# Kernel optimization log

Measured on AMD Instinct MI355X. Metric: run time of the kernel, lower is better.

## Reference

```python
import jax, jax.numpy as jnp
import numpy as np

N = 10000       # nodes (cells)
NFEAT = 2000    # gene-expression features
NFE = 256       # embed features
NH = 128        # nhid
NHE = 64        # nhid_embed
L = 2           # gcn_hid_layers_num
NOUT = 20       # output classes
BN_EPS = 1e-5


def bn_eval(x, g, b, rm, rv):
    # BatchNorm1d in eval mode: affine with running stats
    return g * (x - rm) / jnp.sqrt(rv + BN_EPS) + b


def lstm_layer(seq, Wih, Whh, bih, bhh):
    # seq: [T, N, H_in]; PyTorch gate order i, f, g, o
    Hd = Whh.shape[1]
    def step(carry, xt):
        h, c = carry
        z = xt @ Wih.T + h @ Whh.T + bih + bhh  # [N, 4H]
        i, f, g, o = jnp.split(z, 4, axis=1)
        c = jax.nn.sigmoid(f) * c + jax.nn.sigmoid(i) * jnp.tanh(g)
        h = jax.nn.sigmoid(o) * jnp.tanh(c)
        return (h, c), h
    h0 = jnp.zeros((seq.shape[1], Hd), seq.dtype)
    _, hs = jax.lax.scan(step, (h0, h0), seq)
    return hs  # [T, N, H]


def setup_inputs() -> dict:
    key = jax.random.key(0)
    ks = iter(jax.random.split(key, 48))
    def rn(shape, scale=1.0):
        return jax.random.normal(next(ks), shape, dtype=jnp.float32) * scale
    inp = {}
    inp["x"] = rn((N, NFEAT))
    inp["embed"] = rn((N, NFE))
    inp["adj"] = jax.random.uniform(next(ks), (N, N), dtype=jnp.float32)
    inp["W_in"] = rn((NH, NFEAT), NFEAT ** -0.5); inp["b_in"] = jnp.zeros((NH,), jnp.float32)
    inp["bn_in_g"] = jnp.ones((NH,), jnp.float32); inp["bn_in_b"] = jnp.zeros((NH,), jnp.float32)
    inp["bn_in_rm"] = rn((NH,), 0.1); inp["bn_in_rv"] = jnp.ones((NH,), jnp.float32)
    # gs_block: Linear(2*nhid -> nhid) per layer (concat self + mean-aggregated neighbors)
    inp["W_gs"] = rn((L, NH, 2 * NH), (2 * NH) ** -0.5); inp["b_gs"] = jnp.zeros((L, NH), jnp.float32)
    for l in range(2):  # 2-layer LSTM jumping-knowledge
        inp[f"Wih{l}"] = rn((4 * NH, NH), NH ** -0.5)
        inp[f"Whh{l}"] = rn((4 * NH, NH), NH ** -0.5)
        inp[f"bih{l}"] = jnp.zeros((4 * NH,), jnp.float32)
        inp[f"bhh{l}"] = jnp.zeros((4 * NH,), jnp.float32)
    inp["W_emb"] = rn((NHE, NFE), NFE ** -0.5); inp["b_emb"] = jnp.zeros((NHE,), jnp.float32)
    inp["bn_emb_g"] = jnp.ones((NHE,), jnp.float32); inp["bn_emb_b"] = jnp.zeros((NHE,), jnp.float32)
    inp["bn_emb_rm"] = rn((NHE,), 0.1); inp["bn_emb_rv"] = jnp.ones((NHE,), jnp.float32)
    D = NH + NHE
    inp["W_fc"] = rn((D, D), D ** -0.5); inp["b_fc"] = jnp.zeros((D,), jnp.float32)
    inp["bn_fc_g"] = jnp.ones((D,), jnp.float32); inp["bn_fc_b"] = jnp.zeros((D,), jnp.float32)
    inp["bn_fc_rm"] = rn((D,), 0.1); inp["bn_fc_rv"] = jnp.ones((D,), jnp.float32)
    inp["W_out"] = rn((NOUT, D), D ** -0.5); inp["b_out"] = jnp.zeros((NOUT,), jnp.float32)
    return inp


def _forward(x, embed, adj, W_in, b_in, bn_in_g, bn_in_b, bn_in_rm, bn_in_rv,
             W_gs, b_gs, Wih0, Whh0, bih0, bhh0, Wih1, Whh1, bih1, bhh1,
             W_emb, b_emb, bn_emb_g, bn_emb_b, bn_emb_rm, bn_emb_rv,
             W_fc, b_fc, bn_fc_g, bn_fc_b, bn_fc_rm, bn_fc_rv, W_out, b_out):
    # input projection + BN + ELU (dropout: eval mode -> no-op)
    h = jax.nn.elu(bn_eval(x @ W_in.T + b_in, bn_in_g, bn_in_b, bn_in_rm, bn_in_rv))
    # GraphSAGE mean aggregator: row-normalized dense adjacency
    adj_norm = adj / adj.sum(1, keepdims=True)
    jk = []
    for l in range(L):
        neigh = adj_norm @ h                              # [N, NH] neighbor mean
        comb = jnp.concatenate([h, neigh], axis=1)        # [N, 2NH] (gcn=False)
        h = jax.nn.relu(comb @ W_gs[l].T + b_gs[l])
        h = h / jnp.maximum(jnp.linalg.norm(h, axis=1, keepdims=True), 1e-12)  # F.normalize
        jk.append(h)
    seq = jnp.stack(jk, 0)                                # [L, N, NH]
    hs = lstm_layer(seq, Wih0, Whh0, bih0, bhh0)
    hs = lstm_layer(hs, Wih1, Whh1, bih1, bhh1)
    h = hs.mean(0)                                        # JK: mean of LSTM outputs
    h = jax.nn.elu(bn_eval(h, bn_in_g, bn_in_b, bn_in_rm, bn_in_rv))  # bn_node_in_exp reused
    e = jax.nn.elu(bn_eval(embed @ W_emb.T + b_emb, bn_emb_g, bn_emb_b, bn_emb_rm, bn_emb_rv))
    h = jnp.concatenate([h, e], axis=1)                   # [N, NH+NHE]
    h = jax.nn.elu(bn_eval(h @ W_fc.T + b_fc, bn_fc_g, bn_fc_b, bn_fc_rm, bn_fc_rv))
    logits = h @ W_out.T + b_out
    return jax.nn.log_softmax(logits, axis=1)


def reference(x, embed, adj, W_in, b_in, bn_in_g, bn_in_b, bn_in_rm, bn_in_rv,
              W_gs, b_gs, Wih0, Whh0, bih0, bhh0, Wih1, Whh1, bih1, bhh1,
              W_emb, b_emb, bn_emb_g, bn_emb_b, bn_emb_rm, bn_emb_rv,
              W_fc, b_fc, bn_fc_g, bn_fc_b, bn_fc_rm, bn_fc_rv, W_out, b_out):
    return _forward(x, embed, adj, W_in, b_in, bn_in_g, bn_in_b, bn_in_rm, bn_in_rv,
                    W_gs, b_gs, Wih0, Whh0, bih0, bhh0, Wih1, Whh1, bih1, bhh1,
                    W_emb, b_emb, bn_emb_g, bn_emb_b, bn_emb_rm, bn_emb_rv,
                    W_fc, b_fc, bn_fc_g, bn_fc_b, bn_fc_rm, bn_fc_rv, W_out, b_out)
```

## Files before the change

kernel.cpp:

```cpp
#include <hip/hip_runtime.h>
#include <hip/hip_bf16.h>
#include <math.h>

#define N_NODES 10000
#define NFEAT   2000
#define NFE     256
#define NH      128
#define NHE     64
#define NOUT    20
#define DCAT    192
#define BN_EPS  1e-5f

#define KP      10016
#define KSTEPS  313
#define MT      157
#define NSPLIT  8
#define KC      40
#define NSPLX   4
#define MPAD    10048

typedef __attribute__((ext_vector_type(8))) short  bf16x8;
typedef __attribute__((ext_vector_type(4))) float  f32x4;

__device__ __forceinline__ float sigm(float x) { return 1.0f / (1.0f + expf(-x)); }

__device__ __forceinline__ unsigned short f2bf(float x) {
    union { __hip_bfloat16 h; unsigned short u; } c;
    c.h = __float2bfloat16(x);
    return c.u;
}

__device__ __forceinline__ bf16x8 cvt8(const float* v) {
    bf16x8 r;
    #pragma unroll
    for (int i = 0; i < 8; ++i) r[i] = (short)f2bf(v[i]);
    return r;
}

__global__ __launch_bounds__(256) void wconv_kernel(const float* __restrict__ Wih0,
                                                    const float* __restrict__ Whh0,
                                                    const float* __restrict__ Wih1,
                                                    const float* __restrict__ Whh1,
                                                    const float* __restrict__ Wgs,
                                                    unsigned short* __restrict__ wl,
                                                    unsigned short* __restrict__ wgb)
{
    const int total = 262144 + 65536;
    for (int i = blockIdx.x * 256 + threadIdx.x; i < total; i += gridDim.x * 256) {
        if (i < 262144) {
            int l = i >> 17, rem = i & 131071;
            int n = rem >> 8, k = rem & 255;
            const float* src;
            if (l == 0) src = (k < 128) ? (Wih0 + n * 128 + k) : (Whh0 + n * 128 + (k - 128));
            else        src = (k < 128) ? (Wih1 + n * 128 + k) : (Whh1 + n * 128 + (k - 128));
            wl[i] = f2bf(*src);
        } else {
            int j = i - 262144;
            wgb[j] = f2bf(Wgs[j]);
        }
    }
}

__global__ __launch_bounds__(256) void adjmm_kernel(const float* __restrict__ adj,
                                                    const unsigned short* __restrict__ hT,
                                                    float* __restrict__ part,
                                                    float* __restrict__ part_s)
{
    __shared__ unsigned short sa[2][64 * 32];
    __shared__ unsigned short sb[2][128 * 32];
    const int tid  = threadIdx.x;
    const int lane = tid & 63, w = tid >> 6;
    const int m0   = blockIdx.x * 64;
    const int ks0  = blockIdx.y * KC;
    const int ks1  = min(ks0 + KC, KSTEPS);
    const int r0   = (w & 1) * 32;
    const int c0   = (w >> 1) * 64;

    const int arow = tid >> 2, agrp = tid & 3;
    const size_t abase = (size_t)min(m0 + arow, N_NODES - 1) * N_NODES;
    const int bcol = tid >> 1, bg0 = (tid & 1) * 2;

    const int asoff  = arow * 32 + ((agrp ^ (arow & 3)) << 3);
    const int bsoff0 = bcol * 32 + (((bg0 + 0) ^ (bcol & 3)) << 3);
    const int bsoff1 = bcol * 32 + (((bg0 + 1) ^ (bcol & 3)) << 3);

    float rs = 0.f;
    f32x4 acc[2][4];
    #pragma unroll
    for (int i = 0; i < 2; ++i)
        #pragma unroll
        for (int j = 0; j < 4; ++j) acc[i][j] = (f32x4){0.f, 0.f, 0.f, 0.f};

    float av8[8];
    bf16x8 vb0, vb1;
    auto load_step = [&](int ks) {
        const int k0 = ks * 32;
        const int kg = k0 + agrp * 8;
        if (kg + 8 <= N_NODES) {
            float4 u0 = *(const float4*)(adj + abase + kg);
            float4 u1 = *(const float4*)(adj + abase + kg + 4);
            av8[0] = u0.x; av8[1] = u0.y; av8[2] = u0.z; av8[3] = u0.w;
            av8[4] = u1.x; av8[5] = u1.y; av8[6] = u1.z; av8[7] = u1.w;
        } else {
            #pragma unroll
            for (int i = 0; i < 8; ++i) av8[i] = 0.f;
        }
        #pragma unroll
        for (int i = 0; i < 8; ++i) rs += av8[i];
        vb0 = *(const bf16x8*)(hT + (size_t)bcol * KP + k0 + bg0 * 8);
        vb1 = *(const bf16x8*)(hT + (size_t)bcol * KP + k0 + (bg0 + 1) * 8);
    };
    auto write_step = [&](int p) {
        *(bf16x8*)(sa[p] + asoff)  = cvt8(av8);
        *(bf16x8*)(sb[p] + bsoff0) = vb0;
        *(bf16x8*)(sb[p] + bsoff1) = vb1;
    };

    load_step(ks0);
    write_step(0);

    for (int ks = ks0; ks < ks1; ++ks) {
        const int p = (ks - ks0) & 1;
        const bool more = (ks + 1 < ks1);
        if (more) load_step(ks + 1);
        __syncthreads();
        bf16x8 av[2], bv[4];
        #pragma unroll
        for (int rb = 0; rb < 2; ++rb) {
            int row = r0 + rb * 16 + (lane & 15);
            int g   = lane >> 4;
            av[rb] = *(const bf16x8*)(sa[p] + row * 32 + ((g ^ (row & 3)) << 3));
        }
        #pragma unroll
        for (int cb = 0; cb < 4; ++cb) {
            int col = c0 + cb * 16 + (lane & 15);
            int g   = lane >> 4;
            bv[cb] = *(const bf16x8*)(sb[p] + col * 32 + ((g ^ (col & 3)) << 3));
        }
        #pragma unroll
        for (int rb = 0; rb < 2; ++rb)
            #pragma unroll
            for (int cb = 0; cb < 4; ++cb)
                acc[rb][cb] = __builtin_amdgcn_mfma_f32_16x16x32_bf16(av[rb], bv[cb],
                                                                      acc[rb][cb], 0, 0, 0);
        if (more) write_step(p ^ 1);
    }

    rs += __shfl_xor(rs, 1);
    rs += __shfl_xor(rs, 2);
    if ((tid & 3) == 0) part_s[(size_t)blockIdx.y * MPAD + m0 + arow] = rs;

    float* pout = part + (size_t)blockIdx.y * MPAD * NH;
    #pragma unroll
    for (int rb = 0; rb < 2; ++rb)
        #pragma unroll
        for (int cb = 0; cb < 4; ++cb) {
            int rowb = m0 + r0 + rb * 16 + (lane >> 4) * 4;
            int col  = c0 + cb * 16 + (lane & 15);
            #pragma unroll
            for (int reg = 0; reg < 4; ++reg)
                pout[(size_t)(rowb + reg) * NH + col] = acc[rb][cb][reg];
        }
}

__global__ __launch_bounds__(256) void xw_mfma_kernel(const float* __restrict__ x,
                                                      const float* __restrict__ Wn,
                                                      float* __restrict__ part)
{
    __shared__ unsigned short sa[2][64 * 32];
    __shared__ unsigned short sb[2][128 * 32];
    const int tid  = threadIdx.x;
    const int lane = tid & 63, w = tid >> 6;
    const int m0   = blockIdx.x * 64;
    const int TOT  = (NFEAT + 31) / 32;
    const int s0   = blockIdx.y * 16;
    const int s1   = min(s0 + 16, TOT);
    const int r0   = (w & 1) * 32;
    const int c0   = (w >> 1) * 64;

    const int arow = tid >> 2, agrp = tid & 3;
    const size_t abase = (size_t)min(m0 + arow, N_NODES - 1) * NFEAT;
    const int asoff = arow * 32 + ((agrp ^ (arow & 3)) << 3);
    const int bn0 = tid >> 2;
    int bn_[2], bgrp_[2], bsoff_[2];
    #pragma unroll
    for (int t = 0; t < 2; ++t) {
        int gi = tid + t * 256;
        bn_[t] = gi >> 2; bgrp_[t] = gi & 3;
        bsoff_[t] = bn_[t] * 32 + ((bgrp_[t] ^ (bn_[t] & 3)) << 3);
    }

    f32x4 acc[2][4];
    #pragma unroll
    for (int i = 0; i < 2; ++i)
        #pragma unroll
        for (int j = 0; j < 4; ++j) acc[i][j] = (f32x4){0.f, 0.f, 0.f, 0.f};

    float av8[8], bv8[2][8];
    auto load_step = [&](int ks) {
        const int k0 = ks * 32;
        {
            const int kg = k0 + agrp * 8;
            if (kg + 8 <= NFEAT) {
                float4 u0 = *(const float4*)(x + abase + kg);
                float4 u1 = *(const float4*)(x + abase + kg + 4);
                av8[0]=u0.x; av8[1]=u0.y; av8[2]=u0.z; av8[3]=u0.w;
                av8[4]=u1.x; av8[5]=u1.y; av8[6]=u1.z; av8[7]=u1.w;
            } else {
                #pragma unroll
                for (int i = 0; i < 8; ++i) av8[i] = 0.f;
            }
        }
        #pragma unroll
        for (int t = 0; t < 2; ++t) {
            int kg = k0 + bgrp_[t] * 8;
            if (kg + 8 <= NFEAT) {
                float4 u0 = *(const float4*)(Wn + (size_t)bn_[t] * NFEAT + kg);
                float4 u1 = *(const float4*)(Wn + (size_t)bn_[t] * NFEAT + kg + 4);
                bv8[t][0]=u0.x; bv8[t][1]=u0.y; bv8[t][2]=u0.z; bv8[t][3]=u0.w;
                bv8[t][4]=u1.x; bv8[t][5]=u1.y; bv8[t][6]=u1.z; bv8[t][7]=u1.w;
            } else {
                #pragma unroll
                for (int i = 0; i < 8; ++i) bv8[t][i] = 0.f;
            }
        }
    };
    auto write_step = [&](int p) {
        *(bf16x8*)(sa[p] + asoff) = cvt8(av8);
        #pragma unroll
        for (int t = 0; t < 2; ++t)
            *(bf16x8*)(sb[p] + bsoff_[t]) = cvt8(bv8[t]);
    };

    load_step(s0);
    write_step(0);

    for (int ks = s0; ks < s1; ++ks) {
        const int p = (ks - s0) & 1;
        const bool more = (ks + 1 < s1);
        if (more) load_step(ks + 1);
        __syncthreads();
        bf16x8 av[2], bv[4];
        #pragma unroll
        for (int rb = 0; rb < 2; ++rb) {
            int row = r0 + rb * 16 + (lane & 15);
            int g   = lane >> 4;
            av[rb] = *(const bf16x8*)(sa[p] + row * 32 + ((g ^ (row & 3)) << 3));
        }
        #pragma unroll
        for (int cb = 0; cb < 4; ++cb) {
            int col = c0 + cb * 16 + (lane & 15);
            int g   = lane >> 4;
            bv[cb] = *(const bf16x8*)(sb[p] + col * 32 + ((g ^ (col & 3)) << 3));
        }
        #pragma unroll
        for (int rb = 0; rb < 2; ++rb)
            #pragma unroll
            for (int cb = 0; cb < 4; ++cb)
                acc[rb][cb] = __builtin_amdgcn_mfma_f32_16x16x32_bf16(av[rb], bv[cb],
                                                                      acc[rb][cb], 0, 0, 0);
        if (more) write_step(p ^ 1);
    }
    float* pout = part + (size_t)blockIdx.y * MPAD * NH;
    #pragma unroll
    for (int rb = 0; rb < 2; ++rb)
        #pragma unroll
        for (int cb = 0; cb < 4; ++cb) {
            int rowb = m0 + r0 + rb * 16 + (lane >> 4) * 4;
            int col  = c0 + cb * 16 + (lane & 15);
            #pragma unroll
            for (int reg = 0; reg < 4; ++reg)
                pout[(size_t)(rowb + reg) * NH + col] = acc[rb][cb][reg];
        }
}

__global__ __launch_bounds__(256) void xw_reduce_kernel(const float* __restrict__ part,
                                                        const float* __restrict__ bias,
                                                        const float* __restrict__ g,
                                                        const float* __restrict__ bb,
                                                        const float* __restrict__ rm,
                                                        const float* __restrict__ rv,
                                                        float* __restrict__ h,
                                                        unsigned short* __restrict__ hT)
{
    __shared__ unsigned short tb[128][8];
    const int tid = threadIdx.x;
    int idx = blockIdx.x * 256 + tid;
    const int c4 = (tid & 31) * 4;
    const int lr = tid >> 5;
    const int m0g = blockIdx.x * 8;
    const size_t ch = (size_t)MPAD * NH / 4;
    const float4* p = (const float4*)part;
    float a[4] = {0.f, 0.f, 0.f, 0.f};
    #pragma unroll
    for (int c = 0; c < NSPLX; ++c) {
        float4 v = p[c * ch + idx];
        a[0] += v.x; a[1] += v.y; a[2] += v.z; a[3] += v.w;
    }
    float o[4];
    #pragma unroll
    for (int j = 0; j < 4; ++j) {
        int c = c4 + j;
        float sc = g[c] / sqrtf(rv[c] + BN_EPS);
        float t = (a[j] + bias[c] - rm[c]) * sc + bb[c];
        o[j] = t > 0.f ? t : expm1f(t);
        tb[c][lr] = f2bf(o[j]);
    }
    float4 ov; ov.x = o[0]; ov.y = o[1]; ov.z = o[2]; ov.w = o[3];
    *(float4*)(h + (size_t)idx * 4) = ov;
    __syncthreads();
    if (tid < 128) {
        ushort4 v0, v1;
        v0.x = tb[tid][0]; v0.y = tb[tid][1]; v0.z = tb[tid][2]; v0.w = tb[tid][3];
        v1.x = tb[tid][4]; v1.y = tb[tid][5]; v1.z = tb[tid][6]; v1.w = tb[tid][7];
        *(ushort4*)(hT + (size_t)tid * KP + m0g)     = v0;
        *(ushort4*)(hT + (size_t)tid * KP + m0g + 4) = v1;
        if (blockIdx.x == 0) {
            ushort4 zz; zz.x = zz.y = zz.z = zz.w = 0;
            #pragma unroll
            for (int q = 0; q < 4; ++q)
                *(ushort4*)(hT + (size_t)tid * KP + 10000 + q * 4) = zz;
        }
    }
}

template<bool WRITE_T>
__global__ __launch_bounds__(256) void gs_fused_kernel(const float* __restrict__ h,
                                                       const float* __restrict__ part,
                                                       const float* __restrict__ part_s,
                                                       const unsigned short* __restrict__ Wg,
                                                       const float* __restrict__ bg,
                                                       float* __restrict__ jk,
                                                       unsigned short* __restrict__ jkT)
{
    __shared__ unsigned short sa[64 * 32];
    __shared__ unsigned short sb[128 * 32];
    __shared__ float ssq_l[64][2];
    __shared__ unsigned short tb[WRITE_T ? 128 * 64 : 1];
    const int tid  = threadIdx.x;
    const int lane = tid & 63, w = tid >> 6;
    const int m0   = blockIdx.x * 64;
    const int r0   = (w & 1) * 32;
    const int c0   = (w >> 1) * 64;
    const int arow = tid >> 2, agrp = tid & 3;
    const int mg   = min(m0 + arow, N_NODES - 1);

    float inv;
    {
        float s = 0.f;
        #pragma unroll
        for (int c = 0; c < NSPLIT; ++c) s += part_s[(size_t)c * MPAD + mg];
        inv = 1.0f / s;
    }

    f32x4 acc[2][4];
    #pragma unroll
    for (int i = 0; i < 2; ++i)
        #pragma unroll
        for (int j = 0; j < 4; ++j) acc[i][j] = (f32x4){0.f, 0.f, 0.f, 0.f};

    for (int k0 = 0; k0 < 256; k0 += 32) {
        const int kg = k0 + agrp * 8;
        float a8[8];
        if (kg < 128) {
            const float* asrc = h + (size_t)mg * NH + kg;
            float4 u0 = *(const float4*)asrc;
            float4 u1 = *(const float4*)(asrc + 4);
            a8[0]=u0.x; a8[1]=u0.y; a8[2]=u0.z; a8[3]=u0.w;
            a8[4]=u1.x; a8[5]=u1.y; a8[6]=u1.z; a8[7]=u1.w;
        } else {
            const int cc = kg - 128;
            float s0x=0,s0y=0,s0z=0,s0w=0,s1x=0,s1y=0,s1z=0,s1w=0;
            #pragma unroll
            for (int c = 0; c < NSPLIT; ++c) {
                const float* pp = part + (size_t)c * MPAD * NH + (size_t)mg * NH + cc;
                float4 v0 = *(const float4*)pp;
                float4 v1 = *(const float4*)(pp + 4);
                s0x+=v0.x; s0y+=v0.y; s0z+=v0.z; s0w+=v0.w;
                s1x+=v1.x; s1y+=v1.y; s1z+=v1.z; s1w+=v1.w;
            }
            a8[0]=s0x*inv; a8[1]=s0y*inv; a8[2]=s0z*inv; a8[3]=s0w*inv;
            a8[4]=s1x*inv; a8[5]=s1y*inv; a8[6]=s1z*inv; a8[7]=s1w*inv;
        }
        bf16x8 b8[2];
        #pragma unroll
        for (int t = 0; t < 2; ++t) {
            int gi = tid + t * 256;
            int n = gi >> 2, grp = gi & 3;
            b8[t] = *(const bf16x8*)(Wg + (size_t)n * 256 + k0 + grp * 8);
        }
        __syncthreads();
        *(bf16x8*)(sa + arow * 32 + ((agrp ^ (arow & 3)) << 3)) = cvt8(a8);
        #pragma unroll
        for (int t = 0; t < 2; ++t) {
            int gi = tid + t * 256;
            int n = gi >> 2, grp = gi & 3;
            *(bf16x8*)(sb + n * 32 + ((grp ^ (n & 3)) << 3)) = b8[t];
        }
        __syncthreads();
        bf16x8 av[2], bv[4];
        #pragma unroll
        for (int rb = 0; rb < 2; ++rb) {
            int row = r0 + rb * 16 + (lane & 15);
            int g   = lane >> 4;
            av[rb] = *(const bf16x8*)(sa + row * 32 + ((g ^ (row & 3)) << 3));
        }
        #pragma unroll
        for (int cb = 0; cb < 4; ++cb) {
            int col = c0 + cb * 16 + (lane & 15);
            int g   = lane >> 4;
            bv[cb] = *(const bf16x8*)(sb + col * 32 + ((g ^ (col & 3)) << 3));
        }
        #pragma unroll
        for (int rb = 0; rb < 2; ++rb)
            #pragma unroll
            for (int cb = 0; cb < 4; ++cb)
                acc[rb][cb] = __builtin_amdgcn_mfma_f32_16x16x32_bf16(av[rb], bv[cb],
                                                                      acc[rb][cb], 0, 0, 0);
    }

    float vv[2][4][4];
    float ps[2][4] = {};
    #pragma unroll
    for (int rb = 0; rb < 2; ++rb)
        #pragma unroll
        for (int cb = 0; cb < 4; ++cb) {
            int colg = c0 + cb * 16 + (lane & 15);
            float b = bg[colg];
            #pragma unroll
            for (int reg = 0; reg < 4; ++reg) {
                float t = fmaxf(acc[rb][cb][reg] + b, 0.f);
                vv[rb][cb][reg] = t;
                ps[rb][reg] += t * t;
            }
        }
    #pragma unroll
    for (int msk = 1; msk < 16; msk <<= 1)
        #pragma unroll
        for (int rb = 0; rb < 2; ++rb)
            #pragma unroll
            for (int reg = 0; reg < 4; ++reg)
                ps[rb][reg] += __shfl_xor(ps[rb][reg], msk);
    if ((lane & 15) == 0) {
        #pragma unroll
        for (int rb = 0; rb < 2; ++rb)
            #pragma unroll
            for (int reg = 0; reg < 4; ++reg)
                ssq_l[r0 + rb * 16 + (lane >> 4) * 4 + reg][w >> 1] = ps[rb][reg];
    }
    __syncthreads();
    #pragma unroll
    for (int rb = 0; rb < 2; ++rb)
        #pragma unroll
        for (int reg = 0; reg < 4; ++reg) {
            int lr = r0 + rb * 16 + (lane >> 4) * 4 + reg;
            float s = ssq_l[lr][0] + ssq_l[lr][1];
            float sc = 1.0f / fmaxf(sqrtf(s), 1e-12f);
            int m = m0 + lr;
            #pragma unroll
            for (int cb = 0; cb < 4; ++cb) {
                int colg = c0 + cb * 16 + (lane & 15);
                float o = vv[rb][cb][reg] * sc;
                if (m < N_NODES) jk[(size_t)m * NH + colg] = o;
                if constexpr (WRITE_T) tb[colg * 64 + lr] = f2bf(o);
            }
        }
    if constexpr (WRITE_T) {
        __syncthreads();
        #pragma unroll
        for (int p = 0; p < 4; ++p) {
            int flat = (tid + p * 256) * 8;
            int c = flat >> 6, mo = flat & 63;
            int kglob = m0 + mo;
            if (kglob < KP) {
                unsigned short tmp[8];
                #pragma unroll
                for (int i = 0; i < 8; ++i)
                    tmp[i] = (kglob + i < N_NODES) ? tb[c * 64 + mo + i] : (unsigned short)0;
                ushort4 v0, v1;
                v0.x = tmp[0]; v0.y = tmp[1]; v0.z = tmp[2]; v0.w = tmp[3];
                v1.x = tmp[4]; v1.y = tmp[5]; v1.z = tmp[6]; v1.w = tmp[7];
                *(ushort4*)(jkT + (size_t)c * KP + kglob)     = v0;
                *(ushort4*)(jkT + (size_t)c * KP + kglob + 4) = v1;
            }
        }
    }
}

template<bool HASC, bool FINAL>
__global__ __launch_bounds__(256) void lstm_fused_kernel(
    int K, const float* __restrict__ a1, const float* __restrict__ a2,
    const unsigned short* __restrict__ wl,
    const float* __restrict__ bih, const float* __restrict__ bhh,
    const float* __restrict__ cprev,
    float* __restrict__ hout, float* __restrict__ cout,
    const float* __restrict__ hmean, const float* __restrict__ bng,
    const float* __restrict__ bnb, const float* __restrict__ bnrm,
    const float* __restrict__ bnrv, float* __restrict__ hpost)
{
    __shared__ unsigned short sa[32 * 32];
    __shared__ unsigned short sb[512 * 32];
    const int tid  = threadIdx.x;
    const int lane = tid & 63, w = tid >> 6;
    const int m0   = blockIdx.x * 32;
    const int arow = tid >> 2, agrp = tid & 3;
    const int mg   = min(m0 + arow, N_NODES - 1);

    f32x4 acc[2][8];
    #pragma unroll
    for (int i = 0; i < 2; ++i)
        #pragma unroll
        for (int j = 0; j < 8; ++j) acc[i][j] = (f32x4){0.f, 0.f, 0.f, 0.f};

    for (int k0 = 0; k0 < K; k0 += 32) {
        float a8[8];
        if (tid < 128) {
            int kg = k0 + agrp * 8;
            const float* asrc = (kg < 128) ? (a1 + (size_t)mg * NH + kg)
                                           : (a2 + (size_t)mg * NH + (kg - 128));
            float4 u0 = *(const float4*)asrc;
            float4 u1 = *(const float4*)(asrc + 4);
            a8[0]=u0.x; a8[1]=u0.y; a8[2]=u0.z; a8[3]=u0.w;
            a8[4]=u1.x; a8[5]=u1.y; a8[6]=u1.z; a8[7]=u1.w;
        }
        bf16x8 b8[8];
        #pragma unroll
        for (int t = 0; t < 8; ++t) {
            int gi = tid + t * 256;
            int n = gi >> 2, grp = gi & 3;
            b8[t] = *(const bf16x8*)(wl + (size_t)n * 256 + k0 + grp * 8);
        }
        __syncthreads();
        if (tid < 128)
            *(bf16x8*)(sa + arow * 32 + ((agrp ^ (arow & 3)) << 3)) = cvt8(a8);
        #pragma unroll
        for (int t = 0; t < 8; ++t) {
            int gi = tid + t * 256;
            int n = gi >> 2, grp = gi & 3;
            *(bf16x8*)(sb + n * 32 + ((grp ^ (n & 3)) << 3)) = b8[t];
        }
        __syncthreads();
        bf16x8 av[2];
        #pragma unroll
        for (int rb = 0; rb < 2; ++rb) {
            int row = rb * 16 + (lane & 15);
            int g   = lane >> 4;
            av[rb] = *(const bf16x8*)(sa + row * 32 + ((g ^ (row & 3)) << 3));
        }
        #pragma unroll
        for (int gate = 0; gate < 4; ++gate)
            #pragma unroll
            for (int cb = 0; cb < 2; ++cb) {
                int col = gate * 128 + w * 32 + cb * 16 + (lane & 15);
                int g   = lane >> 4;
                bf16x8 bv = *(const bf16x8*)(sb + col * 32 + ((g ^ (col & 3)) << 3));
                #pragma unroll
                for (int rb = 0; rb < 2; ++rb)
                    acc[rb][gate * 2 + cb] =
                        __builtin_amdgcn_mfma_f32_16x16x32_bf16(av[rb], bv,
                                                                acc[rb][gate * 2 + cb], 0, 0, 0);
            }
    }

    #pragma unroll
    for (int cb = 0; cb < 2; ++cb) {
        const int cg = w * 32 + cb * 16 + (lane & 15);
        const float bi = bih[0 * 128 + cg] + bhh[0 * 128 + cg];
        const float bf = bih[1 * 128 + cg] + bhh[1 * 128 + cg];
        const float bgg= bih[2 * 128 + cg] + bhh[2 * 128 + cg];
        const float bo = bih[3 * 128 + cg] + bhh[3 * 128 + cg];
        float sc = 0.f, sh = 0.f;
        if constexpr (FINAL) {
            sc = bng[cg] / sqrtf(bnrv[cg] + BN_EPS);
            sh = bnb[cg] - bnrm[cg] * sc;
        }
        #pragma unroll
        for (int rb = 0; rb < 2; ++rb) {
            #pragma unroll
            for (int reg = 0; reg < 4; ++reg) {
                int m = m0 + rb * 16 + (lane >> 4) * 4 + reg;
                if (m < N_NODES) {
                    float zi = acc[rb][0 + cb][reg] + bi;
                    float zf = acc[rb][2 + cb][reg] + bf;
                    float zg = acc[rb][4 + cb][reg] + bgg;
                    float zo = acc[rb][6 + cb][reg] + bo;
                    float cn = sigm(zi) * tanhf(zg);
                    if constexpr (HASC) cn += sigm(zf) * cprev[(size_t)m * NH + cg];
                    float hv = sigm(zo) * tanhf(cn);
                    if constexpr (FINAL) {
                        float t = 0.5f * (hmean[(size_t)m * NH + cg] + hv);
                        t = t * sc + sh;
                        hpost[(size_t)m * NH + cg] = t > 0.f ? t : expm1f(t);
                    } else {
                        hout[(size_t)m * NH + cg] = hv;
                        cout[(size_t)m * NH + cg] = cn;
                    }
                }
            }
        }
    }
}

template<int BM, int BN>
__global__ __launch_bounds__(256) void wgemm_bnelu_kernel(
    int M, int K, int kSplitA,
    const float* __restrict__ a1, int lda1,
    const float* __restrict__ a2, int lda2,
    const float* __restrict__ B, int ldb, int ncol,
    float* __restrict__ out, int ldo,
    const float* __restrict__ bias,
    const float* __restrict__ bng, const float* __restrict__ bnb,
    const float* __restrict__ bnrm, const float* __restrict__ bnrv)
{
    constexpr int WC = BN / 64;
    constexpr int WR = 4 / WC;
    static_assert(WR * WC == 4 && BM == WR * 32, "geometry");
    constexpr int NGA = BM * 4 / 256;
    constexpr int NGB = BN * 4 / 256;
    __shared__ unsigned short sa[BM * 32];
    __shared__ unsigned short sb[BN * 32];
    const int tid  = threadIdx.x;
    const int lane = tid & 63, w = tid >> 6;
    const int m0   = blockIdx.x * BM, n0 = blockIdx.y * BN;
    const int r0   = (w % WR) * 32, c0 = (w / WR) * 64;

    f32x4 acc[2][4];
    #pragma unroll
    for (int i = 0; i < 2; ++i)
        #pragma unroll
        for (int j = 0; j < 4; ++j) acc[i][j] = (f32x4){0.f, 0.f, 0.f, 0.f};

    for (int k0 = 0; k0 < K; k0 += 32) {
        float ar[NGA][8], br[NGB][8];
        #pragma unroll
        for (int t = 0; t < NGA; ++t) {
            int gi = tid + t * 256;
            int row = gi >> 2, grp = gi & 3;
            int mg = min(m0 + row, M - 1);
            int kg = k0 + grp * 8;
            const float* src = (kg < kSplitA) ? (a1 + (size_t)mg * lda1 + kg)
                                              : (a2 + (size_t)mg * lda2 + (kg - kSplitA));
            float4 u0 = *(const float4*)src;
            float4 u1 = *(const float4*)(src + 4);
            ar[t][0]=u0.x; ar[t][1]=u0.y; ar[t][2]=u0.z; ar[t][3]=u0.w;
            ar[t][4]=u1.x; ar[t][5]=u1.y; ar[t][6]=u1.z; ar[t][7]=u1.w;
        }
        #pragma unroll
        for (int t = 0; t < NGB; ++t) {
            int gi = tid + t * 256;
            int n = gi >> 2, grp = gi & 3;
            int ng = min(n0 + n, ncol - 1);
            int kg = k0 + grp * 8;
            const float* src = B + (size_t)ng * ldb + kg;
            float4 u0 = *(const float4*)src;
            float4 u1 = *(const float4*)(src + 4);
            br[t][0]=u0.x; br[t][1]=u0.y; br[t][2]=u0.z; br[t][3]=u0.w;
            br[t][4]=u1.x; br[t][5]=u1.y; br[t][6]=u1.z; br[t][7]=u1.w;
        }
        __syncthreads();
        #pragma unroll
        for (int t = 0; t < NGA; ++t) {
            int gi = tid + t * 256;
            int row = gi >> 2, grp = gi & 3;
            *(bf16x8*)(sa + row * 32 + ((grp ^ (row & 3)) << 3)) = cvt8(ar[t]);
        }
        #pragma unroll
        for (int t = 0; t < NGB; ++t) {
            int gi = tid + t * 256;
            int n = gi >> 2, grp = gi & 3;
            *(bf16x8*)(sb + n * 32 + ((grp ^ (n & 3)) << 3)) = cvt8(br[t]);
        }
        __syncthreads();
        bf16x8 av[2], bv[4];
        #pragma unroll
        for (int rb = 0; rb < 2; ++rb) {
            int row = r0 + rb * 16 + (lane & 15);
            int g   = lane >> 4;
            av[rb] = *(const bf16x8*)(sa + row * 32 + ((g ^ (row & 3)) << 3));
        }
        #pragma unroll
        for (int cb = 0; cb < 4; ++cb) {
            int col = c0 + cb * 16 + (lane & 15);
            int g   = lane >> 4;
            bv[cb] = *(const bf16x8*)(sb + col * 32 + ((g ^ (col & 3)) << 3));
        }
        #pragma unroll
        for (int rb = 0; rb < 2; ++rb)
            #pragma unroll
            for (int cb = 0; cb < 4; ++cb)
                acc[rb][cb] = __builtin_amdgcn_mfma_f32_16x16x32_bf16(av[rb], bv[cb],
                                                                      acc[rb][cb], 0, 0, 0);
    }

    #pragma unroll
    for (int cb = 0; cb < 4; ++cb) {
        const int colg = n0 + c0 + cb * 16 + (lane & 15);
        const int cc = min(colg, ncol - 1);
        float badd = bias[cc];
        float sc = bng[cc] / sqrtf(bnrv[cc] + BN_EPS);
        float sh = bnb[cc] - bnrm[cc] * sc;
        #pragma unroll
        for (int rb = 0; rb < 2; ++rb) {
            int rowb = m0 + r0 + rb * 16 + (lane >> 4) * 4;
            #pragma unroll
            for (int reg = 0; reg < 4; ++reg) {
                int m = rowb + reg;
                if (m < M && colg < ncol) {
                    float t = (acc[rb][cb][reg] + badd) * sc + sh;
                    out[(size_t)m * ldo + colg] = t > 0.f ? t : expm1f(t);
                }
            }
        }
    }
}

__global__ __launch_bounds__(256) void out_kernel(const float* __restrict__ hfc,
                                                  const float* __restrict__ W_out,
                                                  const float* __restrict__ b_out,
                                                  float* __restrict__ out)
{
    __shared__ float wl[NOUT * 193];
    __shared__ float rl[4][DCAT];
    const int tid = threadIdx.x;
    for (int i = tid; i < NOUT * DCAT; i += 256)
        wl[(i / DCAT) * 193 + (i % DCAT)] = W_out[i];
    const int w = tid >> 6, lane = tid & 63;
    const int r = blockIdx.x * 4 + w;
    for (int k = lane; k < DCAT; k += 64) rl[w][k] = hfc[(size_t)r * DCAT + k];
    __syncthreads();
    const int c = lane;
    float acc = -INFINITY;
    if (c < NOUT) {
        acc = b_out[c];
        #pragma unroll 4
        for (int k = 0; k < DCAT; ++k) acc += rl[w][k] * wl[c * 193 + k];
    }
    float mx = acc;
    #pragma unroll
    for (int msk = 16; msk >= 1; msk >>= 1) mx = fmaxf(mx, __shfl_xor(mx, msk));
    float ex = (c < NOUT) ? expf(acc - mx) : 0.f;
    float sm = ex;
    #pragma unroll
    for (int msk = 16; msk >= 1; msk >>= 1) sm += __shfl_xor(sm, msk);
    if (c < NOUT) out[(size_t)r * NOUT + c] = acc - mx - logf(sm);
}

extern "C" void kernel_launch(void* const* d_in, const int* in_sizes, int n_in,
                              void* d_out, int out_size, void* d_ws, size_t ws_size,
                              hipStream_t stream)
{
    const float* x       = (const float*)d_in[0];
    const float* embed   = (const float*)d_in[1];
    const float* adj     = (const float*)d_in[2];
    const float* W_in    = (const float*)d_in[3];
    const float* b_in    = (const float*)d_in[4];
    const float* bn_in_g = (const float*)d_in[5];
    const float* bn_in_b = (const float*)d_in[6];
    const float* bn_in_rm= (const float*)d_in[7];
    const float* bn_in_rv= (const float*)d_in[8];
    const float* W_gs    = (const float*)d_in[9];
    const float* b_gs    = (const float*)d_in[10];
    const float* Wih0    = (const float*)d_in[11];
    const float* Whh0    = (const float*)d_in[12];
    const float* bih0    = (const float*)d_in[13];
    const float* bhh0    = (const float*)d_in[14];
    const float* Wih1    = (const float*)d_in[15];
    const float* Whh1    = (const float*)d_in[16];
    const float* bih1    = (const float*)d_in[17];
    const float* bhh1    = (const float*)d_in[18];
    const float* W_emb   = (const float*)d_in[19];
    const float* b_emb   = (const float*)d_in[20];
    const float* bn_e_g  = (const float*)d_in[21];
    const float* bn_e_b  = (const float*)d_in[22];
    const float* bn_e_rm = (const float*)d_in[23];
    const float* bn_e_rv = (const float*)d_in[24];
    const float* W_fc    = (const float*)d_in[25];
    const float* b_fc    = (const float*)d_in[26];
    const float* bn_f_g  = (const float*)d_in[27];
    const float* bn_f_b  = (const float*)d_in[28];
    const float* bn_f_rm = (const float*)d_in[29];
    const float* bn_f_rv = (const float*)d_in[30];
    const float* W_out   = (const float*)d_in[31];
    const float* b_out   = (const float*)d_in[32];
    float* outp = (float*)d_out;

    const size_t HB = (size_t)N_NODES * NH * sizeof(float);
    char* wp = (char*)d_ws;
    auto carve = [&](size_t bytes) {
        void* p = (void*)wp;
        wp += (bytes + 1023) & ~(size_t)1023;
        return p;
    };
    float* part  = (float*)carve((size_t)NSPLIT * MPAD * NH * sizeof(float));
    float* part_s= (float*)carve((size_t)NSPLIT * MPAD * sizeof(float));
    float* h_in  = (float*)carve(HB);
    float* jk0   = (float*)carve(HB);
    float* jk1   = (float*)carve(HB);
    float* h1_0  = (float*)carve(HB);
    float* h1_1  = (float*)carve(HB);
    float* c1    = (float*)carve(HB);
    float* h2_0  = (float*)carve(HB);
    float* c2    = (float*)carve(HB);
    float* hpost = (float*)carve(HB);
    float* e     = (float*)carve((size_t)N_NODES * NHE * sizeof(float));
    float* hfc   = (float*)carve((size_t)N_NODES * DCAT * sizeof(float));
    unsigned short* hT  = (unsigned short*)carve((size_t)NH * KP * 2);
    unsigned short* wl  = (unsigned short*)carve((size_t)2 * 512 * 256 * 2);
    unsigned short* wgb = (unsigned short*)carve((size_t)2 * 128 * 256 * 2);
    if ((size_t)(wp - (char*)d_ws) > ws_size) return;

    const dim3 blk(256);

    wconv_kernel<<<320, blk, 0, stream>>>(Wih0, Whh0, Wih1, Whh1, W_gs, wl, wgb);

    xw_mfma_kernel<<<dim3(MT, NSPLX), blk, 0, stream>>>(x, W_in, part);
    xw_reduce_kernel<<<1250, blk, 0, stream>>>(part, b_in, bn_in_g, bn_in_b,
                                               bn_in_rm, bn_in_rv, h_in, hT);

    adjmm_kernel<<<dim3(MT, NSPLIT), blk, 0, stream>>>(adj, hT, part, part_s);
    gs_fused_kernel<true><<<MT, blk, 0, stream>>>(h_in, part, part_s, wgb, b_gs, jk0, hT);

    adjmm_kernel<<<dim3(MT, NSPLIT), blk, 0, stream>>>(adj, hT, part, part_s);
    gs_fused_kernel<false><<<MT, blk, 0, stream>>>(jk0, part, part_s, wgb + 128 * 256,
                                                   b_gs + 128, jk1, nullptr);

    lstm_fused_kernel<false, false><<<313, blk, 0, stream>>>(
        128, jk0, jk0, wl, bih0, bhh0, nullptr, h1_0, c1,
        nullptr, nullptr, nullptr, nullptr, nullptr, nullptr);
    lstm_fused_kernel<true, false><<<313, blk, 0, stream>>>(
        256, jk1, h1_0, wl, bih0, bhh0, c1, h1_1, c1,
        nullptr, nullptr, nullptr, nullptr, nullptr, nullptr);
    lstm_fused_kernel<false, false><<<313, blk, 0, stream>>>(
        128, h1_0, h1_0, wl + 512 * 256, bih1, bhh1, nullptr, h2_0, c2,
        nullptr, nullptr, nullptr, nullptr, nullptr, nullptr);
    lstm_fused_kernel<true, true><<<313, blk, 0, stream>>>(
        256, h1_1, h2_0, wl + 512 * 256, bih1, bhh1, c2, nullptr, nullptr,
        h2_0, bn_in_g, bn_in_b, bn_in_rm, bn_in_rv, hpost);

    wgemm_bnelu_kernel<64, 128><<<dim3(MT, 1), blk, 0, stream>>>(
        N_NODES, NFE, NFE, embed, NFE, nullptr, 0,
        W_emb, NFE, NHE, e, NHE,
        b_emb, bn_e_g, bn_e_b, bn_e_rm, bn_e_rv);

    wgemm_bnelu_kernel<64, 128><<<dim3(MT, 2), blk, 0, stream>>>(
        N_NODES, DCAT, NH, hpost, NH, e, NHE,
        W_fc, DCAT, DCAT, hfc, DCAT,
        b_fc, bn_f_g, bn_f_b, bn_f_rm, bn_f_rv);

    out_kernel<<<2500, blk, 0, stream>>>(hfc, W_out, b_out, outp);
}
```

Before: 476.9 us.

## Fuse LSTM chain and epilogue GEMMs, store adj partials in bf16, double K-splits

The four LSTM step launches become one kernel that keeps hidden states in LDS as bf16 and cell states in registers, so the h/c intermediates no longer round-trip through global memory. The embed GEMM, FC GEMM and output log-softmax are merged into a single epilogue kernel. The adj-matmul split-K partials are now written in bf16 with twice as many K-splits, which halves the bytes per partial and raises parallelism. In exchange, partial sums are rounded to bf16 before reduction, which costs some precision, and the fused kernels use more shared memory, which may lower occupancy.

Measured after the change: 475.4 us. About the same (-0.3%).

```diff
diff --git a/kernel.cpp b/kernel.cpp
--- a/kernel.cpp
+++ b/kernel.cpp
@@ -14,8 +14,8 @@
 #define KP      10016
 #define KSTEPS  313
 #define MT      157
-#define NSPLIT  8
-#define KC      40
+#define NSPLIT  16
+#define KC      20
 #define NSPLX   4
 #define MPAD    10048
 
@@ -28,6 +28,12 @@
     union { __hip_bfloat16 h; unsigned short u; } c;
     c.h = __float2bfloat16(x);
     return c.u;
+}
+
+__device__ __forceinline__ float bf2f(unsigned short u) {
+    union { float f; unsigned int i; } c;
+    c.i = ((unsigned int)u) << 16;
+    return c.f;
 }
 
 __device__ __forceinline__ bf16x8 cvt8(const float* v) {
@@ -63,7 +69,7 @@
 
 __global__ __launch_bounds__(256) void adjmm_kernel(const float* __restrict__ adj,
                                                     const unsigned short* __restrict__ hT,
-                                                    float* __restrict__ part,
+                                                    unsigned short* __restrict__ part,
                                                     float* __restrict__ part_s)
 {
     __shared__ unsigned short sa[2][64 * 32];
@@ -105,12 +111,12 @@
             #pragma unroll
             for (int i = 0; i < 8; ++i) av8[i] = 0.f;
         }
-        #pragma unroll
-        for (int i = 0; i < 8; ++i) rs += av8[i];
         vb0 = *(const bf16x8*)(hT + (size_t)bcol * KP + k0 + bg0 * 8);
         vb1 = *(const bf16x8*)(hT + (size_t)bcol * KP + k0 + (bg0 + 1) * 8);
     };
     auto write_step = [&](int p) {
+        #pragma unroll
+        for (int i = 0; i < 8; ++i) rs += av8[i];
         *(bf16x8*)(sa[p] + asoff)  = cvt8(av8);
         *(bf16x8*)(sb[p] + bsoff0) = vb0;
         *(bf16x8*)(sb[p] + bsoff1) = vb1;
@@ -150,7 +156,7 @@
     rs += __shfl_xor(rs, 2);
     if ((tid & 3) == 0) part_s[(size_t)blockIdx.y * MPAD + m0 + arow] = rs;
 
-    float* pout = part + (size_t)blockIdx.y * MPAD * NH;
+    unsigned short* pout = part + (size_t)blockIdx.y * MPAD * NH;
     #pragma unroll
     for (int rb = 0; rb < 2; ++rb)
         #pragma unroll
@@ -159,7 +165,7 @@
             int col  = c0 + cb * 16 + (lane & 15);
             #pragma unroll
             for (int reg = 0; reg < 4; ++reg)
-                pout[(size_t)(rowb + reg) * NH + col] = acc[rb][cb][reg];
+                pout[(size_t)(rowb + reg) * NH + col] = f2bf(acc[rb][cb][reg]);
         }
 }
 
@@ -181,7 +187,6 @@
     const int arow = tid >> 2, agrp = tid & 3;
     const size_t abase = (size_t)min(m0 + arow, N_NODES - 1) * NFEAT;
     const int asoff = arow * 32 + ((agrp ^ (arow & 3)) << 3);
-    const int bn0 = tid >> 2;
     int bn_[2], bgrp_[2], bsoff_[2];
     #pragma unroll
     for (int t = 0; t < 2; ++t) {
@@ -326,7 +331,7 @@
 
 template<bool WRITE_T>
 __global__ __launch_bounds__(256) void gs_fused_kernel(const float* __restrict__ h,
-                                                       const float* __restrict__ part,
+                                                       const unsigned short* __restrict__ part,
                                                        const float* __restrict__ part_s,
                                                        const unsigned short* __restrict__ Wg,
                                                        const float* __restrict__ bg,
@@ -370,17 +375,15 @@
             a8[4]=u1.x; a8[5]=u1.y; a8[6]=u1.z; a8[7]=u1.w;
         } else {
             const int cc = kg - 128;
-            float s0x=0,s0y=0,s0z=0,s0w=0,s1x=0,s1y=0,s1z=0,s1w=0;
+            float s[8] = {0.f,0.f,0.f,0.f,0.f,0.f,0.f,0.f};
             #pragma unroll
             for (int c = 0; c < NSPLIT; ++c) {
-                const float* pp = part + (size_t)c * MPAD * NH + (size_t)mg * NH + cc;
-                float4 v0 = *(const float4*)pp;
-                float4 v1 = *(const float4*)(pp + 4);
-                s0x+=v0.x; s0y+=v0.y; s0z+=v0.z; s0w+=v0.w;
-                s1x+=v1.x; s1y+=v1.y; s1z+=v1.z; s1w+=v1.w;
-            }
-            a8[0]=s0x*inv; a8[1]=s0y*inv; a8[2]=s0z*inv; a8[3]=s0w*inv;
-            a8[4]=s1x*inv; a8[5]=s1y*inv; a8[6]=s1z*inv; a8[7]=s1w*inv;
+                bf16x8 v = *(const bf16x8*)(part + (size_t)c * MPAD * NH + (size_t)mg * NH + cc);
+                #pragma unroll
+                for (int i = 0; i < 8; ++i) s[i] += bf2f((unsigned short)v[i]);
+            }
+            #pragma unroll
+            for (int i = 0; i < 8; ++i) a8[i] = s[i] * inv;
         }
         bf16x8 b8[2];
         #pragma unroll
@@ -487,262 +490,335 @@
     }
 }
 
-template<bool HASC, bool FINAL>
-__global__ __launch_bounds__(256) void lstm_fused_kernel(
-    int K, const float* __restrict__ a1, const float* __restrict__ a2,
+__global__ __launch_bounds__(256) void lstm4_kernel(
+    const float* __restrict__ jk0, const float* __restrict__ jk1,
     const unsigned short* __restrict__ wl,
-    const float* __restrict__ bih, const float* __restrict__ bhh,
-    const float* __restrict__ cprev,
-    float* __restrict__ hout, float* __restrict__ cout,
-    const float* __restrict__ hmean, const float* __restrict__ bng,
-    const float* __restrict__ bnb, const float* __restrict__ bnrm,
-    const float* __restrict__ bnrv, float* __restrict__ hpost)
+    const float* __restrict__ bih0, const float* __restrict__ bhh0,
+    const float* __restrict__ bih1, const float* __restrict__ bhh1,
+    const float* __restrict__ bng, const float* __restrict__ bnb,
+    const float* __restrict__ bnrm, const float* __restrict__ bnrv,
+    float* __restrict__ hpost)
 {
     __shared__ unsigned short sa[32 * 32];
     __shared__ unsigned short sb[512 * 32];
-    const int tid  = threadIdx.x;
-    const int lane = tid & 63, w = tid >> 6;
-    const int m0   = blockIdx.x * 32;
+    __shared__ unsigned short hb[2][32][136];
+    const int tid = threadIdx.x, lane = tid & 63, w = tid >> 6;
+    const int m0 = blockIdx.x * 32;
     const int arow = tid >> 2, agrp = tid & 3;
-    const int mg   = min(m0 + arow, N_NODES - 1);
+    const int mg = min(m0 + arow, N_NODES - 1);
 
     f32x4 acc[2][8];
-    #pragma unroll
-    for (int i = 0; i < 2; ++i)
-        #pragma unroll
-        for (int j = 0; j < 8; ++j) acc[i][j] = (f32x4){0.f, 0.f, 0.f, 0.f};
-
-    for (int k0 = 0; k0 < K; k0 += 32) {
-        float a8[8];
+    float cst[2][2][4];
+
+    auto zacc = [&] {
+        #pragma unroll
+        for (int i = 0; i < 2; ++i)
+            #pragma unroll
+            for (int j = 0; j < 8; ++j) acc[i][j] = (f32x4){0.f, 0.f, 0.f, 0.f};
+    };
+    auto stage_sb = [&](const unsigned short* wlayer, int k0) {
+        #pragma unroll
+        for (int t = 0; t < 8; ++t) {
+            int gi = tid + t * 256, n = gi >> 2, grp = gi & 3;
+            *(bf16x8*)(sb + n * 32 + ((grp ^ (n & 3)) << 3)) =
+                *(const bf16x8*)(wlayer + (size_t)n * 256 + k0 + grp * 8);
+        }
+    };
+    auto stage_sa = [&](const float* a, int k0) {
         if (tid < 128) {
             int kg = k0 + agrp * 8;
-            const float* asrc = (kg < 128) ? (a1 + (size_t)mg * NH + kg)
-                                           : (a2 + (size_t)mg * NH + (kg - 128));
-            float4 u0 = *(const float4*)asrc;
-            float4 u1 = *(const float4*)(asrc + 4);
-            a8[0]=u0.x; a8[1]=u0.y; a8[2]=u0.z; a8[3]=u0.w;
-            a8[4]=u1.x; a8[5]=u1.y; a8[6]=u1.z; a8[7]=u1.w;
-        }
-        bf16x8 b8[8];
-        #pragma unroll
-        for (int t = 0; t < 8; ++t) {
-            int gi = tid + t * 256;
-            int n = gi >> 2, grp = gi & 3;
-            b8[t] = *(const bf16x8*)(wl + (size_t)n * 256 + k0 + grp * 8);
-        }
-        __syncthreads();
-        if (tid < 128)
+            const float* src = a + (size_t)mg * NH + kg;
+            float4 u0 = *(const float4*)src, u1 = *(const float4*)(src + 4);
+            float a8[8] = {u0.x, u0.y, u0.z, u0.w, u1.x, u1.y, u1.z, u1.w};
             *(bf16x8*)(sa + arow * 32 + ((agrp ^ (arow & 3)) << 3)) = cvt8(a8);
-        #pragma unroll
-        for (int t = 0; t < 8; ++t) {
-            int gi = tid + t * 256;
-            int n = gi >> 2, grp = gi & 3;
-            *(bf16x8*)(sb + n * 32 + ((grp ^ (n & 3)) << 3)) = b8[t];
-        }
-        __syncthreads();
-        bf16x8 av[2];
-        #pragma unroll
-        for (int rb = 0; rb < 2; ++rb) {
-            int row = rb * 16 + (lane & 15);
-            int g   = lane >> 4;
-            av[rb] = *(const bf16x8*)(sa + row * 32 + ((g ^ (row & 3)) << 3));
-        }
+        }
+    };
+    auto av_sa = [&](int rb) {
+        int row = rb * 16 + (lane & 15), g = lane >> 4;
+        return *(const bf16x8*)(sa + row * 32 + ((g ^ (row & 3)) << 3));
+    };
+    auto av_hb = [&](int i, int rb, int kl) {
+        int row = rb * 16 + (lane & 15), g = lane >> 4;
+        return *(const bf16x8*)(&hb[i][row][kl + g * 8]);
+    };
+    auto mfma_all = [&](bf16x8 a0, bf16x8 a1) {
         #pragma unroll
         for (int gate = 0; gate < 4; ++gate)
             #pragma unroll
             for (int cb = 0; cb < 2; ++cb) {
                 int col = gate * 128 + w * 32 + cb * 16 + (lane & 15);
-                int g   = lane >> 4;
+                int g = lane >> 4;
                 bf16x8 bv = *(const bf16x8*)(sb + col * 32 + ((g ^ (col & 3)) << 3));
+                acc[0][gate * 2 + cb] =
+                    __builtin_amdgcn_mfma_f32_16x16x32_bf16(a0, bv, acc[0][gate * 2 + cb], 0, 0, 0);
+                acc[1][gate * 2 + cb] =
+                    __builtin_amdgcn_mfma_f32_16x16x32_bf16(a1, bv, acc[1][gate * 2 + cb], 0, 0, 0);
+            }
+    };
+    auto epi = [&](const float* bih, const float* bhh, bool hasc, int hdst, bool fin) {
+        __syncthreads();
+        #pragma unroll
+        for (int cb = 0; cb < 2; ++cb) {
+            int cg = w * 32 + cb * 16 + (lane & 15);
+            float bi  = bih[cg]       + bhh[cg];
+            float bf_ = bih[128 + cg] + bhh[128 + cg];
+            float bgg = bih[256 + cg] + bhh[256 + cg];
+            float bo  = bih[384 + cg] + bhh[384 + cg];
+            float sc = 0.f, sh = 0.f;
+            if (fin) {
+                sc = bng[cg] / sqrtf(bnrv[cg] + BN_EPS);
+                sh = bnb[cg] - bnrm[cg] * sc;
+            }
+            #pragma unroll
+            for (int rb = 0; rb < 2; ++rb)
                 #pragma unroll
-                for (int rb = 0; rb < 2; ++rb)
-                    acc[rb][gate * 2 + cb] =
-                        __builtin_amdgcn_mfma_f32_16x16x32_bf16(av[rb], bv,
-                                                                acc[rb][gate * 2 + cb], 0, 0, 0);
-            }
-    }
-
-    #pragma unroll
-    for (int cb = 0; cb < 2; ++cb) {
-        const int cg = w * 32 + cb * 16 + (lane & 15);
-        const float bi = bih[0 * 128 + cg] + bhh[0 * 128 + cg];
-        const float bf = bih[1 * 128 + cg] + bhh[1 * 128 + cg];
-        const float bgg= bih[2 * 128 + cg] + bhh[2 * 128 + cg];
-        const float bo = bih[3 * 128 + cg] + bhh[3 * 128 + cg];
-        float sc = 0.f, sh = 0.f;
-        if constexpr (FINAL) {
-            sc = bng[cg] / sqrtf(bnrv[cg] + BN_EPS);
-            sh = bnb[cg] - bnrm[cg] * sc;
-        }
-        #pragma unroll
-        for (int rb = 0; rb < 2; ++rb) {
-            #pragma unroll
-            for (int reg = 0; reg < 4; ++reg) {
-                int m = m0 + rb * 16 + (lane >> 4) * 4 + reg;
-                if (m < N_NODES) {
+                for (int reg = 0; reg < 4; ++reg) {
+                    int lr = rb * 16 + (lane >> 4) * 4 + reg;
                     float zi = acc[rb][0 + cb][reg] + bi;
-                    float zf = acc[rb][2 + cb][reg] + bf;
+                    float zf = acc[rb][2 + cb][reg] + bf_;
                     float zg = acc[rb][4 + cb][reg] + bgg;
                     float zo = acc[rb][6 + cb][reg] + bo;
                     float cn = sigm(zi) * tanhf(zg);
-                    if constexpr (HASC) cn += sigm(zf) * cprev[(size_t)m * NH + cg];
+                    if (hasc) cn += sigm(zf) * cst[rb][cb][reg];
+                    cst[rb][cb][reg] = cn;
                     float hv = sigm(zo) * tanhf(cn);
-                    if constexpr (FINAL) {
-                        float t = 0.5f * (hmean[(size_t)m * NH + cg] + hv);
+                    if (fin) {
+                        float hm = bf2f(hb[0][lr][cg]);
+                        float t = 0.5f * (hm + hv);
                         t = t * sc + sh;
-                        hpost[(size_t)m * NH + cg] = t > 0.f ? t : expm1f(t);
+                        int m = m0 + lr;
+                        if (m < N_NODES) hpost[(size_t)m * NH + cg] = t > 0.f ? t : expm1f(t);
                     } else {
-                        hout[(size_t)m * NH + cg] = hv;
-                        cout[(size_t)m * NH + cg] = cn;
+                        hb[hdst][lr][cg] = f2bf(hv);
                     }
                 }
-            }
-        }
-    }
-}
-
-template<int BM, int BN>
-__global__ __launch_bounds__(256) void wgemm_bnelu_kernel(
-    int M, int K, int kSplitA,
-    const float* __restrict__ a1, int lda1,
-    const float* __restrict__ a2, int lda2,
-    const float* __restrict__ B, int ldb, int ncol,
-    float* __restrict__ out, int ldo,
-    const float* __restrict__ bias,
-    const float* __restrict__ bng, const float* __restrict__ bnb,
-    const float* __restrict__ bnrm, const float* __restrict__ bnrv)
+        }
+        __syncthreads();
+    };
+
+    zacc();
+    for (int k0 = 0; k0 < 128; k0 += 32) {
+        __syncthreads();
+        stage_sa(jk0, k0);
+        stage_sb(wl, k0);
+        __syncthreads();
+        mfma_all(av_sa(0), av_sa(1));
+    }
+    epi(bih0, bhh0, false, 0, false);
+
+    zacc();
+    for (int k0 = 0; k0 < 256; k0 += 32) {
+        __syncthreads();
+        if (k0 < 128) stage_sa(jk1, k0);
+        stage_sb(wl, k0);
+        __syncthreads();
+        if (k0 < 128) mfma_all(av_sa(0), av_sa(1));
+        else          mfma_all(av_hb(0, 0, k0 - 128), av_hb(0, 1, k0 - 128));
+    }
+    epi(bih0, bhh0, true, 1, false);
+
+    const unsigned short* wl1 = wl + 512 * 256;
+    zacc();
+    for (int k0 = 0; k0 < 128; k0 += 32) {
+        __syncthreads();
+        stage_sb(wl1, k0);
+        __syncthreads();
+        mfma_all(av_hb(0, 0, k0), av_hb(0, 1, k0));
+    }
+    epi(bih1, bhh1, false, 0, false);
+
+    zacc();
+    for (int k0 = 0; k0 < 256; k0 += 32) {
+        __syncthreads();
+        stage_sb(wl1, k0);
+        __syncthreads();
+        if (k0 < 128) mfma_all(av_hb(1, 0, k0), av_hb(1, 1, k0));
+        else          mfma_all(av_hb(0, 0, k0 - 128), av_hb(0, 1, k0 - 128));
+    }
+    epi(bih1, bhh1, true, -1, true);
+}
+
+__global__ __launch_bounds__(256) void epilogue_kernel(
+    const float* __restrict__ embed,
+    const float* __restrict__ W_emb, const float* __restrict__ b_emb,
+    const float* __restrict__ bn_e_g, const float* __restrict__ bn_e_b,
+    const float* __restrict__ bn_e_rm, const float* __restrict__ bn_e_rv,
+    const float* __restrict__ hpost,
+    const float* __restrict__ W_fc, const float* __restrict__ b_fc,
+    const float* __restrict__ bn_f_g, const float* __restrict__ bn_f_b,
+    const float* __restrict__ bn_f_rm, const float* __restrict__ bn_f_rv,
+    const float* __restrict__ W_out, const float* __restrict__ b_out,
+    float* __restrict__ out)
 {
-    constexpr int WC = BN / 64;
-    constexpr int WR = 4 / WC;
-    static_assert(WR * WC == 4 && BM == WR * 32, "geometry");
-    constexpr int NGA = BM * 4 / 256;
-    constexpr int NGB = BN * 4 / 256;
-    __shared__ unsigned short sa[BM * 32];
-    __shared__ unsigned short sb[BN * 32];
-    const int tid  = threadIdx.x;
-    const int lane = tid & 63, w = tid >> 6;
-    const int m0   = blockIdx.x * BM, n0 = blockIdx.y * BN;
-    const int r0   = (w % WR) * 32, c0 = (w / WR) * 64;
-
-    f32x4 acc[2][4];
-    #pragma unroll
-    for (int i = 0; i < 2; ++i)
-        #pragma unroll
-        for (int j = 0; j < 4; ++j) acc[i][j] = (f32x4){0.f, 0.f, 0.f, 0.f};
-
-    for (int k0 = 0; k0 < K; k0 += 32) {
-        float ar[NGA][8], br[NGB][8];
-        #pragma unroll
-        for (int t = 0; t < NGA; ++t) {
-            int gi = tid + t * 256;
-            int row = gi >> 2, grp = gi & 3;
-            int mg = min(m0 + row, M - 1);
-            int kg = k0 + grp * 8;
-            const float* src = (kg < kSplitA) ? (a1 + (size_t)mg * lda1 + kg)
-                                              : (a2 + (size_t)mg * lda2 + (kg - kSplitA));
-            float4 u0 = *(const float4*)src;
-            float4 u1 = *(const float4*)(src + 4);
-            ar[t][0]=u0.x; ar[t][1]=u0.y; ar[t][2]=u0.z; ar[t][3]=u0.w;
-            ar[t][4]=u1.x; ar[t][5]=u1.y; ar[t][6]=u1.z; ar[t][7]=u1.w;
-        }
-        #pragma unroll
-        for (int t = 0; t < NGB; ++t) {
-            int gi = tid + t * 256;
-            int n = gi >> 2, grp = gi & 3;
-            int ng = min(n0 + n, ncol - 1);
-            int kg = k0 + grp * 8;
-            const float* src = B + (size_t)ng * ldb + kg;
-            float4 u0 = *(const float4*)src;
-            float4 u1 = *(const float4*)(src + 4);
-            br[t][0]=u0.x; br[t][1]=u0.y; br[t][2]=u0.z; br[t][3]=u0.w;
-            br[t][4]=u1.x; br[t][5]=u1.y; br[t][6]=u1.z; br[t][7]=u1.w;
-        }
-        __syncthreads();
-        #pragma unroll
-        for (int t = 0; t < NGA; ++t) {
-            int gi = tid + t * 256;
-            int row = gi >> 2, grp = gi & 3;
-            *(bf16x8*)(sa + row * 32 + ((grp ^ (row & 3)) << 3)) = cvt8(ar[t]);
-        }
-        #pragma unroll
-        for (int t = 0; t < NGB; ++t) {
-            int gi = tid + t * 256;
-            int n = gi >> 2, grp = gi & 3;
-            *(bf16x8*)(sb + n * 32 + ((grp ^ (n & 3)) << 3)) = cvt8(br[t]);
-        }
-        __syncthreads();
-        bf16x8 av[2], bv[4];
-        #pragma unroll
-        for (int rb = 0; rb < 2; ++rb) {
-            int row = r0 + rb * 16 + (lane & 15);
-            int g   = lane >> 4;
-            av[rb] = *(const bf16x8*)(sa + row * 32 + ((g ^ (row & 3)) << 3));
-        }
+    __shared__ unsigned short sa[64 * 32];
+    __shared__ unsigned short sb[192 * 32];
+    __shared__ unsigned short ebuf[64][72];
+    __shared__ float fbuf[64][204];
+    const int tid = threadIdx.x, lane = tid & 63, w = tid >> 6;
+    const int m0 = blockIdx.x * 64;
+    const int arow = tid >> 2, agrp = tid & 3;
+    const int mg = min(m0 + arow, N_NODES - 1);
+    const int g = lane >> 4;
+
+    f32x4 aE[4];
+    #pragma unroll
+    for (int j = 0; j < 4; ++j) aE[j] = (f32x4){0.f, 0.f, 0.f, 0.f};
+    for (int k0 = 0; k0 < NFE; k0 += 32) {
+        float a8[8], b8[8];
+        {
+            const float* s = embed + (size_t)mg * NFE + k0 + agrp * 8;
+            float4 u0 = *(const float4*)s, u1 = *(const float4*)(s + 4);
+            a8[0]=u0.x; a8[1]=u0.y; a8[2]=u0.z; a8[3]=u0.w;
+            a8[4]=u1.x; a8[5]=u1.y; a8[6]=u1.z; a8[7]=u1.w;
+        }
+        {
+            const float* s = W_emb + (size_t)arow * NFE + k0 + agrp * 8;
+            float4 u0 = *(const float4*)s, u1 = *(const float4*)(s + 4);
+            b8[0]=u0.x; b8[1]=u0.y; b8[2]=u0.z; b8[3]=u0.w;
+            b8[4]=u1.x; b8[5]=u1.y; b8[6]=u1.z; b8[7]=u1.w;
+        }
+        __syncthreads();
+        *(bf16x8*)(sa + arow * 32 + ((agrp ^ (arow & 3)) << 3)) = cvt8(a8);
+        *(bf16x8*)(sb + arow * 32 + ((agrp ^ (arow & 3)) << 3)) = cvt8(b8);
+        __syncthreads();
+        bf16x8 av;
+        { int row = w * 16 + (lane & 15);
+          av = *(const bf16x8*)(sa + row * 32 + ((g ^ (row & 3)) << 3)); }
         #pragma unroll
         for (int cb = 0; cb < 4; ++cb) {
-            int col = c0 + cb * 16 + (lane & 15);
-            int g   = lane >> 4;
-            bv[cb] = *(const bf16x8*)(sb + col * 32 + ((g ^ (col & 3)) << 3));
-        }
-        #pragma unroll
-        for (int rb = 0; rb < 2; ++rb)
-            #pragma unroll
-            for (int cb = 0; cb < 4; ++cb)
-                acc[rb][cb] = __builtin_amdgcn_mfma_f32_16x16x32_bf16(av[rb], bv[cb],
-                                                                      acc[rb][cb], 0, 0, 0);
-    }
-
+            int col = cb * 16 + (lane & 15);
+            bf16x8 bv = *(const bf16x8*)(sb + col * 32 + ((g ^ (col & 3)) << 3));
+            aE[cb] = __builtin_amdgcn_mfma_f32_16x16x32_bf16(av, bv, aE[cb], 0, 0, 0);
+        }
+    }
     #pragma unroll
     for (int cb = 0; cb < 4; ++cb) {
-        const int colg = n0 + c0 + cb * 16 + (lane & 15);
-        const int cc = min(colg, ncol - 1);
-        float badd = bias[cc];
-        float sc = bng[cc] / sqrtf(bnrv[cc] + BN_EPS);
-        float sh = bnb[cc] - bnrm[cc] * sc;
-        #pragma unroll
-        for (int rb = 0; rb < 2; ++rb) {
-            int rowb = m0 + r0 + rb * 16 + (lane >> 4) * 4;
+        int col = cb * 16 + (lane & 15);
+        float sc = bn_e_g[col] / sqrtf(bn_e_rv[col] + BN_EPS);
+        float sh = bn_e_b[col] - bn_e_rm[col] * sc;
+        float bb = b_emb[col];
+        #pragma unroll
+        for (int reg = 0; reg < 4; ++reg) {
+            int row = w * 16 + (lane >> 4) * 4 + reg;
+            float t = (aE[cb][reg] + bb) * sc + sh;
+            ebuf[row][col] = f2bf(t > 0.f ? t : expm1f(t));
+        }
+    }
+    __syncthreads();
+
+    f32x4 aF[4][3];
+    #pragma unroll
+    for (int i = 0; i < 4; ++i)
+        #pragma unroll
+        for (int j = 0; j < 3; ++j) aF[i][j] = (f32x4){0.f, 0.f, 0.f, 0.f};
+    for (int k0 = 0; k0 < DCAT; k0 += 32) {
+        const bool gl = (k0 < 128);
+        float b8[3][8];
+        #pragma unroll
+        for (int t = 0; t < 3; ++t) {
+            int gi = tid + t * 256, n = gi >> 2, grp = gi & 3;
+            const float* s = W_fc + (size_t)n * DCAT + k0 + grp * 8;
+            float4 u0 = *(const float4*)s, u1 = *(const float4*)(s + 4);
+            b8[t][0]=u0.x; b8[t][1]=u0.y; b8[t][2]=u0.z; b8[t][3]=u0.w;
+            b8[t][4]=u1.x; b8[t][5]=u1.y; b8[t][6]=u1.z; b8[t][7]=u1.w;
+        }
+        float a8[8];
+        if (gl) {
+            const float* s = hpost + (size_t)mg * NH + k0 + agrp * 8;
+            float4 u0 = *(const float4*)s, u1 = *(const float4*)(s + 4);
+            a8[0]=u0.x; a8[1]=u0.y; a8[2]=u0.z; a8[3]=u0.w;
+            a8[4]=u1.x; a8[5]=u1.y; a8[6]=u1.z; a8[7]=u1.w;
+        }
+        __syncthreads();
+        if (gl) *(bf16x8*)(sa + arow * 32 + ((agrp ^ (arow & 3)) << 3)) = cvt8(a8);
+        #pragma unroll
+        for (int t = 0; t < 3; ++t) {
+            int gi = tid + t * 256, n = gi >> 2, grp = gi & 3;
+            *(bf16x8*)(sb + n * 32 + ((grp ^ (n & 3)) << 3)) = cvt8(b8[t]);
+        }
+        __syncthreads();
+        #pragma unroll
+        for (int rf = 0; rf < 4; ++rf) {
+            int row = rf * 16 + (lane & 15);
+            bf16x8 av = gl ? *(const bf16x8*)(sa + row * 32 + ((g ^ (row & 3)) << 3))
+                           : *(const bf16x8*)(&ebuf[row][(k0 - 128) + g * 8]);
+            #pragma unroll
+            for (int cf = 0; cf < 3; ++cf) {
+                int col = w * 48 + cf * 16 + (lane & 15);
+                bf16x8 bv = *(const bf16x8*)(sb + col * 32 + ((g ^ (col & 3)) << 3));
+                aF[rf][cf] = __builtin_amdgcn_mfma_f32_16x16x32_bf16(av, bv, aF[rf][cf], 0, 0, 0);
+            }
+        }
+    }
+    #pragma unroll
+    for (int cf = 0; cf < 3; ++cf) {
+        int col = w * 48 + cf * 16 + (lane & 15);
+        float sc = bn_f_g[col] / sqrtf(bn_f_rv[col] + BN_EPS);
+        float sh = bn_f_b[col] - bn_f_rm[col] * sc;
+        float bb = b_fc[col];
+        #pragma unroll
+        for (int rf = 0; rf < 4; ++rf)
             #pragma unroll
             for (int reg = 0; reg < 4; ++reg) {
-                int m = rowb + reg;
-                if (m < M && colg < ncol) {
-                    float t = (acc[rb][cb][reg] + badd) * sc + sh;
-                    out[(size_t)m * ldo + colg] = t > 0.f ? t : expm1f(t);
-                }
-            }
-        }
-    }
-}
-
-__global__ __launch_bounds__(256) void out_kernel(const float* __restrict__ hfc,
-                                                  const float* __restrict__ W_out,
-                                                  const float* __restrict__ b_out,
-                                                  float* __restrict__ out)
-{
-    __shared__ float wl[NOUT * 193];
-    __shared__ float rl[4][DCAT];
-    const int tid = threadIdx.x;
-    for (int i = tid; i < NOUT * DCAT; i += 256)
-        wl[(i / DCAT) * 193 + (i % DCAT)] = W_out[i];
-    const int w = tid >> 6, lane = tid & 63;
-    const int r = blockIdx.x * 4 + w;
-    for (int k = lane; k < DCAT; k += 64) rl[w][k] = hfc[(size_t)r * DCAT + k];
+                int row = rf * 16 + (lane >> 4) * 4 + reg;
+                float t = (aF[rf][cf][reg] + bb) * sc + sh;
+                fbuf[row][col] = t > 0.f ? t : expm1f(t);
+            }
+    }
     __syncthreads();
-    const int c = lane;
-    float acc = -INFINITY;
-    if (c < NOUT) {
-        acc = b_out[c];
-        #pragma unroll 4
-        for (int k = 0; k < DCAT; ++k) acc += rl[w][k] * wl[c * 193 + k];
-    }
-    float mx = acc;
-    #pragma unroll
-    for (int msk = 16; msk >= 1; msk >>= 1) mx = fmaxf(mx, __shfl_xor(mx, msk));
-    float ex = (c < NOUT) ? expf(acc - mx) : 0.f;
-    float sm = ex;
-    #pragma unroll
-    for (int msk = 16; msk >= 1; msk >>= 1) sm += __shfl_xor(sm, msk);
-    if (c < NOUT) out[(size_t)r * NOUT + c] = acc - mx - logf(sm);
+
+    f32x4 aO[2];
+    aO[0] = (f32x4){0.f, 0.f, 0.f, 0.f};
+    aO[1] = (f32x4){0.f, 0.f, 0.f, 0.f};
+    for (int k0 = 0; k0 < DCAT; k0 += 32) {
+        float b8[8];
+        const bool act = tid < 128;
+        if (act) {
+            if (arow < NOUT) {
+                const float* s = W_out + (size_t)arow * DCAT + k0 + agrp * 8;
+                float4 u0 = *(const float4*)s, u1 = *(const float4*)(s + 4);
+                b8[0]=u0.x; b8[1]=u0.y; b8[2]=u0.z; b8[3]=u0.w;
+                b8[4]=u1.x; b8[5]=u1.y; b8[6]=u1.z; b8[7]=u1.w;
+            } else {
+                #pragma unroll
+                for (int i = 0; i < 8; ++i) b8[i] = 0.f;
+            }
+        }
+        __syncthreads();
+        if (act) *(bf16x8*)(sb + arow * 32 + ((agrp ^ (arow & 3)) << 3)) = cvt8(b8);
+        __syncthreads();
+        int row = w * 16 + (lane & 15);
+        float4 f0 = *(const float4*)(&fbuf[row][k0 + g * 8]);
+        float4 f1 = *(const float4*)(&fbuf[row][k0 + g * 8 + 4]);
+        float f8[8] = {f0.x, f0.y, f0.z, f0.w, f1.x, f1.y, f1.z, f1.w};
+        bf16x8 av = cvt8(f8);
+        #pragma unroll
+        for (int cf = 0; cf < 2; ++cf) {
+            int col = cf * 16 + (lane & 15);
+            bf16x8 bv = *(const bf16x8*)(sb + col * 32 + ((g ^ (col & 3)) << 3));
+            aO[cf] = __builtin_amdgcn_mfma_f32_16x16x32_bf16(av, bv, aO[cf], 0, 0, 0);
+        }
+    }
+    const int c0i = lane & 15, c1i = 16 + (lane & 15);
+    const bool v1 = c1i < NOUT;
+    #pragma unroll
+    for (int reg = 0; reg < 4; ++reg) {
+        int row = w * 16 + (lane >> 4) * 4 + reg;
+        int m = m0 + row;
+        float l0 = aO[0][reg] + b_out[c0i];
+        float l1 = v1 ? (aO[1][reg] + b_out[c1i]) : -INFINITY;
+        float mx = fmaxf(l0, l1);
+        #pragma unroll
+        for (int msk = 1; msk < 16; msk <<= 1) mx = fmaxf(mx, __shfl_xor(mx, msk));
+        float s = expf(l0 - mx) + (v1 ? expf(l1 - mx) : 0.f);
+        #pragma unroll
+        for (int msk = 1; msk < 16; msk <<= 1) s += __shfl_xor(s, msk);
+        float lse = mx + logf(s);
+        if (m < N_NODES) {
+            out[(size_t)m * NOUT + c0i] = l0 - lse;
+            if (v1) out[(size_t)m * NOUT + c1i] = l1 - lse;
+        }
+    }
 }
 
 extern "C" void kernel_launch(void* const* d_in, const int* in_sizes, int n_in,
@@ -791,19 +867,14 @@
         wp += (bytes + 1023) & ~(size_t)1023;
         return p;
     };
-    float* part  = (float*)carve((size_t)NSPLIT * MPAD * NH * sizeof(float));
+    void* partRaw = carve((size_t)NSPLIT * MPAD * NH * 2);
+    unsigned short* partB = (unsigned short*)partRaw;
+    float* partF = (float*)partRaw;
     float* part_s= (float*)carve((size_t)NSPLIT * MPAD * sizeof(float));
     float* h_in  = (float*)carve(HB);
     float* jk0   = (float*)carve(HB);
     float* jk1   = (float*)carve(HB);
-    float* h1_0  = (float*)carve(HB);
-    float* h1_1  = (float*)carve(HB);
-    float* c1    = (float*)carve(HB);
-    float* h2_0  = (float*)carve(HB);
-    float* c2    = (float*)carve(HB);
     float* hpost = (float*)carve(HB);
-    float* e     = (float*)carve((size_t)N_NODES * NHE * sizeof(float));
-    float* hfc   = (float*)carve((size_t)N_NODES * DCAT * sizeof(float));
     unsigned short* hT  = (unsigned short*)carve((size_t)NH * KP * 2);
     unsigned short* wl  = (unsigned short*)carve((size_t)2 * 512 * 256 * 2);
     unsigned short* wgb = (unsigned short*)carve((size_t)2 * 128 * 256 * 2);
@@ -813,39 +884,23 @@
 
     wconv_kernel<<<320, blk, 0, stream>>>(Wih0, Whh0, Wih1, Whh1, W_gs, wl, wgb);
 
-    xw_mfma_kernel<<<dim3(MT, NSPLX), blk, 0, stream>>>(x, W_in, part);
-    xw_reduce_kernel<<<1250, blk, 0, stream>>>(part, b_in, bn_in_g, bn_in_b,
+    xw_mfma_kernel<<<dim3(MT, NSPLX), blk, 0, stream>>>(x, W_in, partF);
+    xw_reduce_kernel<<<1250, blk, 0, stream>>>(partF, b_in, bn_in_g, bn_in_b,
                                                bn_in_rm, bn_in_rv, h_in, hT);
 
-    adjmm_kernel<<<dim3(MT, NSPLIT), blk, 0, stream>>>(adj, hT, part, part_s);
-    gs_fused_kernel<true><<<MT, blk, 0, stream>>>(h_in, part, part_s, wgb, b_gs, jk0, hT);
-
-    adjmm_kernel<<<dim3(MT, NSPLIT), blk, 0, stream>>>(adj, hT, part, part_s);
-    gs_fused_kernel<false><<<MT, blk, 0, stream>>>(jk0, part, part_s, wgb + 128 * 256,
+    adjmm_kernel<<<dim3(MT, NSPLIT), blk, 0, stream>>>(adj, hT, partB, part_s);
+    gs_fused_kernel<true><<<MT, blk, 0, stream>>>(h_in, partB, part_s, wgb, b_gs, jk0, hT);
+
+    adjmm_kernel<<<dim3(MT, NSPLIT), blk, 0, stream>>>(adj, hT, partB, part_s);
+    gs_fused_kernel<false><<<MT, blk, 0, stream>>>(jk0, partB, part_s, wgb + 128 * 256,
                                                    b_gs + 128, jk1, nullptr);
 
-    lstm_fused_kernel<false, false><<<313, blk, 0, stream>>>(
-        128, jk0, jk0, wl, bih0, bhh0, nullptr, h1_0, c1,
-        nullptr, nullptr, nullptr, nullptr, nullptr, nullptr);
-    lstm_fused_kernel<true, false><<<313, blk, 0, stream>>>(
-        256, jk1, h1_0, wl, bih0, bhh0, c1, h1_1, c1,
-        nullptr, nullptr, nullptr, nullptr, nullptr, nullptr);
-    lstm_fused_kernel<false, false><<<313, blk, 0, stream>>>(
-        128, h1_0, h1_0, wl + 512 * 256, bih1, bhh1, nullptr, h2_0, c2,
-        nullptr, nullptr, nullptr, nullptr, nullptr, nullptr);
-    lstm_fused_kernel<true, true><<<313, blk, 0, stream>>>(
-        256, h1_1, h2_0, wl + 512 * 256, bih1, bhh1, c2, nullptr, nullptr,
-        h2_0, bn_in_g, bn_in_b, bn_in_rm, bn_in_rv, hpost);
-
-    wgemm_bnelu_kernel<64, 128><<<dim3(MT, 1), blk, 0, stream>>>(
-        N_NODES, NFE, NFE, embed, NFE, nullptr, 0,
-        W_emb, NFE, NHE, e, NHE,
-        b_emb, bn_e_g, bn_e_b, bn_e_rm, bn_e_rv);
-
-    wgemm_bnelu_kernel<64, 128><<<dim3(MT, 2), blk, 0, stream>>>(
-        N_NODES, DCAT, NH, hpost, NH, e, NHE,
-        W_fc, DCAT, DCAT, hfc, DCAT,
-        b_fc, bn_f_g, bn_f_b, bn_f_rm, bn_f_rv);
-
-    out_kernel<<<2500, blk, 0, stream>>>(hfc, W_out, b_out, outp);
-}
+    lstm4_kernel<<<313, blk, 0, stream>>>(jk0, jk1, wl, bih0, bhh0, bih1, bhh1,
+                                          bn_in_g, bn_in_b, bn_in_rm, bn_in_rv, hpost);
+
+    epilogue_kernel<<<MT, blk, 0, stream>>>(embed, W_emb, b_emb,
+                                            bn_e_g, bn_e_b, bn_e_rm, bn_e_rv,
+                                            hpost, W_fc, b_fc,
+                                            bn_f_g, bn_f_b, bn_f_rm, bn_f_rv,
+                                            W_out, b_out, outp);
+}
```
